# Kernel optimization log

Hardware: AMD Instinct MI355X
Metric: run time of the kernel (lower is better)

Reference implementation:

```python
import jax, jax.numpy as jnp
import numpy as np

S, D_IN, H = 8192, 1024, 2048  # seq_len, input dim (vector_sizes[level]), hidden (vector_sizes[level+1])


def setup_inputs() -> dict:
    key = jax.random.key(0)
    k1, k2, k3 = jax.random.split(key, 3)
    inputs = jax.random.normal(k1, (S, D_IN), dtype=jnp.float32)
    W = jax.random.normal(k2, (D_IN, 4 * H), dtype=jnp.float32) * 0.02  # input kernel
    U = jax.random.normal(k3, (H, 4 * H), dtype=jnp.float32) * 0.02    # recurrent kernel
    b = jnp.zeros((4 * H,), dtype=jnp.float32)                          # bias
    return {"inputs": inputs, "W": W, "U": U, "b": b}


def reference(inputs, W, U, b):
    # Keras LSTMCell with activation='linear' (cell/output activation = identity),
    # recurrent_activation = sigmoid, gate order i, f, c, o.
    # RNN(return_sequences=False) -> return last hidden state only.
    h0 = jnp.zeros((H,), dtype=inputs.dtype)
    c0 = jnp.zeros((H,), dtype=inputs.dtype)
    # Precompute input projections for all timesteps: [S, 4H]
    xz = inputs @ W + b

    def step(carry, xz_t):
        h, c = carry
        z = xz_t + h @ U                      # [4H]
        zi, zf, zg, zo = jnp.split(z, 4)
        i = jax.nn.sigmoid(zi)
        f = jax.nn.sigmoid(zf)
        o = jax.nn.sigmoid(zo)
        c_new = f * c + i * zg                # linear candidate activation
        h_new = o * c_new                     # linear output activation
        return (h_new, c_new), None

    (h_last, _), _ = jax.lax.scan(step, (h0, c0), xz)
    return h_last
```

## Files before the change

kernel.cpp:

```cpp
#include <hip/hip_runtime.h>
#include <stdint.h>


#define S_LEN   8192
#define D_INP   1024
#define HDIM    2048
#define FH      8192
#define NWG     256
#define TPB     256
#define XB      8
#define PACE_MAX 120

typedef _Float16 half2_t __attribute__((ext_vector_type(2)));

#if defined(__has_builtin)
#if __has_builtin(__builtin_amdgcn_fdot2)
#define HAVE_FDOT2 1
#endif
#endif

__device__ __forceinline__ float fdot2f(uint32_t a, uint32_t b, float c) {
#ifdef HAVE_FDOT2
    return __builtin_amdgcn_fdot2(__builtin_bit_cast(half2_t, a),
                                  __builtin_bit_cast(half2_t, b), c, false);
#else
    half2_t ha = __builtin_bit_cast(half2_t, a);
    half2_t hb = __builtin_bit_cast(half2_t, b);
    c = fmaf((float)ha.x, (float)hb.x, c);
    c = fmaf((float)ha.y, (float)hb.y, c);
    return c;
#endif
}

__device__ __forceinline__ uint32_t pack2(float a, float b) {
    half2_t h;
    h.x = (_Float16)a;
    h.y = (_Float16)b;
    return __builtin_bit_cast(uint32_t, h);
}

__device__ __forceinline__ float sigmoidf_fast(float z) {
    return 1.0f / (1.0f + __expf(-z));
}

__device__ __forceinline__ unsigned long long ald(const unsigned long long* p) {
    return __hip_atomic_load(p, __ATOMIC_RELAXED, __HIP_MEMORY_SCOPE_AGENT);
}

extern "C" __global__ void __launch_bounds__(TPB, 1)
lstm_persist(const float* __restrict__ x, const float* __restrict__ W,
             const float* __restrict__ U, const float* __restrict__ b,
             float* __restrict__ out, unsigned long long* __restrict__ hbuf)
{
    __shared__ __align__(16) uint32_t xl[XB * 640];
    __shared__ __align__(16) uint32_t hl[32 * 36];
    __shared__ __align__(16) float    zz[4 * 8 * 4];

    const int tid = threadIdx.x;
    const int wg  = blockIdx.x;
    const int cg  = tid & 7;
    const int kc  = tid >> 3;
    const int w   = tid >> 6;

    uint32_t ureg[4][32];
    uint32_t wreg[4][16];
#pragma unroll
    for (int g = 0; g < 4; ++g) {
        const int col = g * HDIM + wg * 8 + cg;
#pragma unroll
        for (int p = 0; p < 32; ++p) {
            const int k0 = kc * 64 + 2 * p;
            ureg[g][p] = pack2(U[(size_t)k0 * FH + col],
                               U[(size_t)(k0 + 1) * FH + col]);
        }
#pragma unroll
        for (int p = 0; p < 16; ++p) {
            const int k0 = kc * 32 + 2 * p;
            wreg[g][p] = pack2(W[(size_t)k0 * FH + col],
                               W[(size_t)(k0 + 1) * FH + col]);
        }
    }
    float bias[4] = {0.f, 0.f, 0.f, 0.f};
    if (tid < 8) {
#pragma unroll
        for (int g = 0; g < 4; ++g) bias[g] = b[g * HDIM + wg * 8 + cg];
    }
    float cst = 0.0f;

    const int xr  = tid >> 5;
    const int kcw = tid & 31;
    float4 pf[8];
    {
        const float4* src = (const float4*)(x + (size_t)xr * D_INP + kcw * 32);
#pragma unroll
        for (int q = 0; q < 8; ++q) pf[q] = src[q];
    }

    unsigned long long* const hb0 = hbuf;
    unsigned long long* const hb1 = hbuf + 1024;

    int pace = 0;

    for (int t = 0; t < S_LEN; ++t) {
        const int s = t & (XB - 1);
        if (s == 0) {
            uint32_t* dst = &xl[xr * 640 + kcw * 20];
#pragma unroll
            for (int q = 0; q < 4; ++q) {
                uint4 v;
                v.x = pack2(pf[2 * q].x, pf[2 * q].y);
                v.y = pack2(pf[2 * q].z, pf[2 * q].w);
                v.z = pack2(pf[2 * q + 1].x, pf[2 * q + 1].y);
                v.w = pack2(pf[2 * q + 1].z, pf[2 * q + 1].w);
                *(uint4*)(dst + q * 4) = v;
            }
            __syncthreads();
            if (t + XB < S_LEN) {
                const float4* src = (const float4*)(
                    x + (size_t)(t + XB + xr) * D_INP + kcw * 32);
#pragma unroll
                for (int q = 0; q < 8; ++q) pf[q] = src[q];
            }
        }

        unsigned long long* const gsrc = ((t & 1) ? hb1 : hb0) + tid * 4;
        unsigned long long a0, a1, a2, a3;
        if (t > 0) {
            for (int i = 0; i < pace; ++i) __builtin_amdgcn_s_sleep(1);
            a0 = ald(gsrc + 0); a1 = ald(gsrc + 1);
            a2 = ald(gsrc + 2); a3 = ald(gsrc + 3);
        }

        float acc[4] = {0.f, 0.f, 0.f, 0.f};
        {
            uint32_t xp[16];
            const uint32_t* xpp = &xl[s * 640 + kc * 20];
            *(uint4*)&xp[0]  = *(const uint4*)(xpp + 0);
            *(uint4*)&xp[4]  = *(const uint4*)(xpp + 4);
            *(uint4*)&xp[8]  = *(const uint4*)(xpp + 8);
            *(uint4*)&xp[12] = *(const uint4*)(xpp + 12);
#pragma unroll
            for (int p = 0; p < 16; ++p) {
#pragma unroll
                for (int g = 0; g < 4; ++g)
                    acc[g] = fdot2f(wreg[g][p], xp[p], acc[g]);
            }
        }

        if (t > 0) {
            const unsigned int want = (unsigned int)t;
            const bool hit = ((unsigned int)(a0 >> 32) == want) &
                             ((unsigned int)(a1 >> 32) == want) &
                             ((unsigned int)(a2 >> 32) == want) &
                             ((unsigned int)(a3 >> 32) == want);
            if (__all(hit)) {
                if (pace > 0) pace -= 1;
            } else {
                pace = (pace + 8 > PACE_MAX) ? PACE_MAX : pace + 8;
                int guard = 0;
                for (;;) {
                    a0 = ald(gsrc + 0); a1 = ald(gsrc + 1);
                    a2 = ald(gsrc + 2); a3 = ald(gsrc + 3);
                    const bool ok = ((unsigned int)(a0 >> 32) == want) &
                                    ((unsigned int)(a1 >> 32) == want) &
                                    ((unsigned int)(a2 >> 32) == want) &
                                    ((unsigned int)(a3 >> 32) == want);
                    if (ok || ++guard >= (1 << 20)) break;
                    __builtin_amdgcn_s_sleep(1);
                }
            }
            uint4 q4;
            q4.x = (unsigned int)a0;
            q4.y = (unsigned int)a1;
            q4.z = (unsigned int)a2;
            q4.w = (unsigned int)a3;
            *(uint4*)&hl[kc * 36 + cg * 4] = q4;
        } else {
            const uint4 z4 = {0u, 0u, 0u, 0u};
            *(uint4*)&hl[kc * 36 + cg * 4] = z4;
        }
        __syncthreads();

        {
            const uint32_t* hp = &hl[kc * 36];
#pragma unroll
            for (int q = 0; q < 8; ++q) {
                const uint4 hv = *(const uint4*)(hp + q * 4);
#pragma unroll
                for (int g = 0; g < 4; ++g) {
                    acc[g] = fdot2f(ureg[g][4 * q + 0], hv.x, acc[g]);
                    acc[g] = fdot2f(ureg[g][4 * q + 1], hv.y, acc[g]);
                    acc[g] = fdot2f(ureg[g][4 * q + 2], hv.z, acc[g]);
                    acc[g] = fdot2f(ureg[g][4 * q + 3], hv.w, acc[g]);
                }
            }
        }

#pragma unroll
        for (int g = 0; g < 4; ++g) {
            acc[g] += __shfl_xor(acc[g], 8);
            acc[g] += __shfl_xor(acc[g], 16);
            acc[g] += __shfl_xor(acc[g], 32);
        }
        if ((tid & 63) < 8) {
            float4 vv = {acc[0], acc[1], acc[2], acc[3]};
            *(float4*)&zz[(w * 8 + cg) * 4] = vv;
        }
        __syncthreads();

        if (tid < 8) {
            const float4 z0 = *(const float4*)&zz[(0 + cg) * 4];
            const float4 z1 = *(const float4*)&zz[(8 + cg) * 4];
            const float4 z2 = *(const float4*)&zz[(16 + cg) * 4];
            const float4 z3 = *(const float4*)&zz[(24 + cg) * 4];
            const float zi = bias[0] + z0.x + z1.x + z2.x + z3.x;
            const float zf = bias[1] + z0.y + z1.y + z2.y + z3.y;
            const float zg = bias[2] + z0.z + z1.z + z2.z + z3.z;
            const float zo = bias[3] + z0.w + z1.w + z2.w + z3.w;
            const float si = sigmoidf_fast(zi);
            const float sf = sigmoidf_fast(zf);
            const float so = sigmoidf_fast(zo);
            const float cn = sf * cst + si * zg;
            cst = cn;
            const float hn = so * cn;
            if (t < S_LEN - 1) {
                const float ha  = __shfl(hn, 2 * cg);
                const float hbv = __shfl(hn, 2 * cg + 1);
                if (cg < 4) {
                    const unsigned long long pv =
                        ((unsigned long long)(unsigned int)(t + 1) << 32) |
                        (unsigned long long)pack2(ha, hbv);
                    unsigned long long* const dst =
                        (((t + 1) & 1) ? hb1 : hb0) + wg * 4 + cg;
                    __hip_atomic_store(dst, pv, __ATOMIC_RELAXED,
                                       __HIP_MEMORY_SCOPE_AGENT);
                }
            } else {
                out[wg * 8 + cg] = hn;
            }
        }
    }
}

extern "C" void kernel_launch(void* const* d_in, const int* in_sizes, int n_in,
                              void* d_out, int out_size, void* d_ws, size_t ws_size,
                              hipStream_t stream) {
    const float* x = (const float*)d_in[0];
    const float* W = (const float*)d_in[1];
    const float* U = (const float*)d_in[2];
    const float* b = (const float*)d_in[3];
    unsigned long long* hbuf = (unsigned long long*)d_ws;

    (void)hipMemsetAsync(hbuf, 0, (size_t)2 * 1024 * sizeof(unsigned long long),
                         stream);

    hipLaunchKernelGGL(lstm_persist, dim3(NWG), dim3(TPB), 0, stream,
                       x, W, U, b, (float*)d_out, hbuf);
}
```

Baseline: 17.94 ms.

## Replace shared-memory h staging with wave shuffles and double-buffer zz

Each thread already loads the h slice that its own 8-lane group needs, so the h values are now broadcast across the group with __shfl instead of being written to LDS. This removes one __syncthreads per timestep. The zz reduction buffer is double-buffered by timestep parity so the next step's writes cannot race with the previous step's reads without an extra barrier. The h atomic loads are issued before the x tile refill so their latency overlaps it, and a single retry is tried before the sleep-poll loop. The cost is 32 shuffles per step in place of 8 LDS uint4 reads.

```diff
diff --git a/kernel.cpp b/kernel.cpp
--- a/kernel.cpp
+++ b/kernel.cpp
@@ -53,14 +53,15 @@
              float* __restrict__ out, unsigned long long* __restrict__ hbuf)
 {
     __shared__ __align__(16) uint32_t xl[XB * 640];
-    __shared__ __align__(16) uint32_t hl[32 * 36];
-    __shared__ __align__(16) float    zz[4 * 8 * 4];
-
-    const int tid = threadIdx.x;
-    const int wg  = blockIdx.x;
-    const int cg  = tid & 7;
-    const int kc  = tid >> 3;
-    const int w   = tid >> 6;
+    __shared__ __align__(16) float    zz[2][4 * 8 * 4];
+
+    const int tid  = threadIdx.x;
+    const int wg   = blockIdx.x;
+    const int cg   = tid & 7;
+    const int kc   = tid >> 3;
+    const int w    = tid >> 6;
+    const int lane = tid & 63;
+    const int gb   = lane & 56;
 
     uint32_t ureg[4][32];
     uint32_t wreg[4][16];
@@ -103,6 +104,15 @@
 
     for (int t = 0; t < S_LEN; ++t) {
         const int s = t & (XB - 1);
+
+        unsigned long long* const gsrc = ((t & 1) ? hb1 : hb0) + tid * 4;
+        unsigned long long a0, a1, a2, a3;
+        if (t > 0) {
+            for (int i = 0; i < pace; ++i) __builtin_amdgcn_s_sleep(1);
+            a0 = ald(gsrc + 0); a1 = ald(gsrc + 1);
+            a2 = ald(gsrc + 2); a3 = ald(gsrc + 3);
+        }
+
         if (s == 0) {
             uint32_t* dst = &xl[xr * 640 + kcw * 20];
 #pragma unroll
@@ -121,14 +131,6 @@
 #pragma unroll
                 for (int q = 0; q < 8; ++q) pf[q] = src[q];
             }
-        }
-
-        unsigned long long* const gsrc = ((t & 1) ? hb1 : hb0) + tid * 4;
-        unsigned long long a0, a1, a2, a3;
-        if (t > 0) {
-            for (int i = 0; i < pace; ++i) __builtin_amdgcn_s_sleep(1);
-            a0 = ald(gsrc + 0); a1 = ald(gsrc + 1);
-            a2 = ald(gsrc + 2); a3 = ald(gsrc + 3);
         }
 
         float acc[4] = {0.f, 0.f, 0.f, 0.f};
@@ -147,52 +149,56 @@
             }
         }
 
+        uint4 q4 = {0u, 0u, 0u, 0u};
         if (t > 0) {
             const unsigned int want = (unsigned int)t;
-            const bool hit = ((unsigned int)(a0 >> 32) == want) &
-                             ((unsigned int)(a1 >> 32) == want) &
-                             ((unsigned int)(a2 >> 32) == want) &
-                             ((unsigned int)(a3 >> 32) == want);
+            bool hit = ((unsigned int)(a0 >> 32) == want) &
+                       ((unsigned int)(a1 >> 32) == want) &
+                       ((unsigned int)(a2 >> 32) == want) &
+                       ((unsigned int)(a3 >> 32) == want);
             if (__all(hit)) {
                 if (pace > 0) pace -= 1;
             } else {
                 pace = (pace + 8 > PACE_MAX) ? PACE_MAX : pace + 8;
-                int guard = 0;
-                for (;;) {
-                    a0 = ald(gsrc + 0); a1 = ald(gsrc + 1);
-                    a2 = ald(gsrc + 2); a3 = ald(gsrc + 3);
-                    const bool ok = ((unsigned int)(a0 >> 32) == want) &
-                                    ((unsigned int)(a1 >> 32) == want) &
-                                    ((unsigned int)(a2 >> 32) == want) &
-                                    ((unsigned int)(a3 >> 32) == want);
-                    if (ok || ++guard >= (1 << 20)) break;
-                    __builtin_amdgcn_s_sleep(1);
+                a0 = ald(gsrc + 0); a1 = ald(gsrc + 1);
+                a2 = ald(gsrc + 2); a3 = ald(gsrc + 3);
+                hit = ((unsigned int)(a0 >> 32) == want) &
+                      ((unsigned int)(a1 >> 32) == want) &
+                      ((unsigned int)(a2 >> 32) == want) &
+                      ((unsigned int)(a3 >> 32) == want);
+                if (!__all(hit)) {
+                    int guard = 0;
+                    for (;;) {
+                        a0 = ald(gsrc + 0); a1 = ald(gsrc + 1);
+                        a2 = ald(gsrc + 2); a3 = ald(gsrc + 3);
+                        const bool ok = ((unsigned int)(a0 >> 32) == want) &
+                                        ((unsigned int)(a1 >> 32) == want) &
+                                        ((unsigned int)(a2 >> 32) == want) &
+                                        ((unsigned int)(a3 >> 32) == want);
+                        if (ok || ++guard >= (1 << 20)) break;
+                        __builtin_amdgcn_s_sleep(1);
+                    }
                 }
             }
-            uint4 q4;
             q4.x = (unsigned int)a0;
             q4.y = (unsigned int)a1;
             q4.z = (unsigned int)a2;
             q4.w = (unsigned int)a3;
-            *(uint4*)&hl[kc * 36 + cg * 4] = q4;
-        } else {
-            const uint4 z4 = {0u, 0u, 0u, 0u};
-            *(uint4*)&hl[kc * 36 + cg * 4] = z4;
-        }
-        __syncthreads();
-
-        {
-            const uint32_t* hp = &hl[kc * 36];
-#pragma unroll
-            for (int q = 0; q < 8; ++q) {
-                const uint4 hv = *(const uint4*)(hp + q * 4);
-#pragma unroll
-                for (int g = 0; g < 4; ++g) {
-                    acc[g] = fdot2f(ureg[g][4 * q + 0], hv.x, acc[g]);
-                    acc[g] = fdot2f(ureg[g][4 * q + 1], hv.y, acc[g]);
-                    acc[g] = fdot2f(ureg[g][4 * q + 2], hv.z, acc[g]);
-                    acc[g] = fdot2f(ureg[g][4 * q + 3], hv.w, acc[g]);
-                }
+        }
+
+#pragma unroll
+        for (int j = 0; j < 8; ++j) {
+            const int sl = gb + j;
+            const uint32_t w0 = __shfl(q4.x, sl);
+            const uint32_t w1 = __shfl(q4.y, sl);
+            const uint32_t w2 = __shfl(q4.z, sl);
+            const uint32_t w3 = __shfl(q4.w, sl);
+#pragma unroll
+            for (int g = 0; g < 4; ++g) {
+                acc[g] = fdot2f(ureg[g][4 * j + 0], w0, acc[g]);
+                acc[g] = fdot2f(ureg[g][4 * j + 1], w1, acc[g]);
+                acc[g] = fdot2f(ureg[g][4 * j + 2], w2, acc[g]);
+                acc[g] = fdot2f(ureg[g][4 * j + 3], w3, acc[g]);
             }
         }
 
@@ -202,17 +208,18 @@
             acc[g] += __shfl_xor(acc[g], 16);
             acc[g] += __shfl_xor(acc[g], 32);
         }
-        if ((tid & 63) < 8) {
+        if (lane < 8) {
             float4 vv = {acc[0], acc[1], acc[2], acc[3]};
-            *(float4*)&zz[(w * 8 + cg) * 4] = vv;
+            *(float4*)&zz[t & 1][(w * 8 + cg) * 4] = vv;
         }
         __syncthreads();
 
         if (tid < 8) {
-            const float4 z0 = *(const float4*)&zz[(0 + cg) * 4];
-            const float4 z1 = *(const float4*)&zz[(8 + cg) * 4];
-            const float4 z2 = *(const float4*)&zz[(16 + cg) * 4];
-            const float4 z3 = *(const float4*)&zz[(24 + cg) * 4];
+            const float* zp = zz[t & 1];
+            const float4 z0 = *(const float4*)&zp[(0 + cg) * 4];
+            const float4 z1 = *(const float4*)&zp[(8 + cg) * 4];
+            const float4 z2 = *(const float4*)&zp[(16 + cg) * 4];
+            const float4 z3 = *(const float4*)&zp[(24 + cg) * 4];
             const float zi = bias[0] + z0.x + z1.x + z2.x + z3.x;
             const float zf = bias[1] + z0.y + z1.y + z2.y + z3.y;
             const float zg = bias[2] + z0.z + z1.z + z2.z + z3.z;
```

Result: slower. 18.48 ms (+3.0%).
